# Performance work log

Hardware: AMD Instinct MI355X
Metric: run time of the kernel (lower is better)

## Reference

```python
import jax, jax.numpy as jnp
import numpy as np

B, S, D = 2, 2048, 1024
H = 16
HD = D // H


def setup_inputs() -> dict:
    key = jax.random.key(0)
    ks = jax.random.split(key, 6)
    X = jax.random.normal(ks[0], (B, S, D), dtype=jnp.float32)
    # Linear weights stored [in, out] so y = x @ W (torch stores transposed).
    sc = 1.0 / np.sqrt(D)
    Wq = jax.random.normal(ks[1], (D, D), dtype=jnp.float32) * sc
    Wk = jax.random.normal(ks[2], (D, D), dtype=jnp.float32) * sc
    Wv = jax.random.normal(ks[3], (D, D), dtype=jnp.float32) * sc
    Wo = jax.random.normal(ks[4], (D, D), dtype=jnp.float32) * sc
    bo = jax.random.normal(ks[5], (D,), dtype=jnp.float32) * 0.01
    return {"X": X, "Wq": Wq, "Wk": Wk, "Wv": Wv, "Wo": Wo, "bo": bo}


def reference(X, Wq, Wk, Wv, Wo, bo):
    b, n, _ = X.shape
    # QKV projections (no bias, qkv_bias=False), reshape to [b, h, n, hd]
    q = (X @ Wq).reshape(b, n, H, HD).transpose(0, 2, 1, 3)
    k = (X @ Wk).reshape(b, n, H, HD).transpose(0, 2, 1, 3)
    v = (X @ Wv).reshape(b, n, H, HD).transpose(0, 2, 1, 3)
    # Unscaled scores (module's scale flag defaults to False)
    scores = jnp.einsum("bhqd,bhkd->bhqk", q, k)
    causal = jnp.triu(jnp.ones((n, n), dtype=bool), k=1)  # True above diagonal
    scores = jnp.where(causal, -jnp.inf, scores)
    attn = jax.nn.softmax(scores, axis=-1)
    # dropout p=0.0 -> identity
    ctx = jnp.einsum("bhqk,bhkd->bqhd", attn, v).reshape(b, n, H * HD)
    return ctx @ Wo + bo
```

## Files before the change

kernel.cpp:

```cpp
#include <hip/hip_runtime.h>
#include <stdint.h>


typedef __attribute__((ext_vector_type(8))) short short8;
typedef __attribute__((ext_vector_type(4))) float floatx4;

#define S_LEN 2048
#define D_DIM 1024
#define NH 16
#define HD 64
#define L2E 1.44269504088896340736f

__device__ __forceinline__ short f2bf(float f) {
    uint32_t u = __builtin_bit_cast(uint32_t, f);
    uint32_t r = u + 0x7fffu + ((u >> 16) & 1u);
    return (short)(r >> 16);
}
__device__ __forceinline__ uint32_t pack2(float a, float b) {
#if __has_builtin(__builtin_amdgcn_cvt_pk_bf16_f32)
    auto v = __builtin_amdgcn_cvt_pk_bf16_f32(a, b);
    uint32_t r; __builtin_memcpy(&r, &v, sizeof(r)); return r;
#else
    return (uint32_t)(uint16_t)f2bf(a) | ((uint32_t)(uint16_t)f2bf(b) << 16);
#endif
}
__device__ __forceinline__ void gll16(const void* g, void* l) {
    __builtin_amdgcn_global_load_lds(
        (const __attribute__((address_space(1))) void*)g,
        (__attribute__((address_space(3))) void*)l, 16, 0, 0);
}

__global__ __launch_bounds__(256) void castx_kernel(const float* __restrict__ X,
                                                    short* __restrict__ Xb) {
    int i = blockIdx.x * 256 + threadIdx.x;
    const float4 v = *(const float4*)(X + (size_t)i * 4);
    uint2 o;
    o.x = pack2(v.x, v.y);
    o.y = pack2(v.z, v.w);
    *(uint2*)(Xb + (size_t)i * 4) = o;
}

__global__ __launch_bounds__(256) void tcast4_kernel(const float* __restrict__ Wq,
                                                     const float* __restrict__ Wk,
                                                     const float* __restrict__ Wv,
                                                     const float* __restrict__ Wo,
                                                     short* __restrict__ WqkvT,
                                                     short* __restrict__ WoT) {
    const int z = blockIdx.z;
    const float* W = (z == 0) ? Wq : (z == 1) ? Wk : (z == 2) ? Wv : Wo;
    short* WT = (z < 3) ? (WqkvT + (size_t)z * 1024 * 1024) : WoT;
    __shared__ float tile[32][33];
    const int bx = blockIdx.x * 32;
    const int by = blockIdx.y * 32;
    const int tx = threadIdx.x, ty = threadIdx.y;
    for (int i = 0; i < 32; i += 8)
        tile[ty + i][tx] = W[(size_t)(bx + ty + i) * D_DIM + by + tx];
    __syncthreads();
    for (int i = 0; i < 32; i += 8)
        WT[(size_t)(by + ty + i) * D_DIM + bx + tx] = f2bf(tile[tx][ty + i]);
}

__device__ __forceinline__ void gemm_main(const short* __restrict__ A,
                                          const short* __restrict__ BT,
                                          short* As, short* Bs,
                                          int m0, int n0, floatx4 (&acc)[4][4],
                                          int tid) {
    const int lane = tid & 63, ln = lane & 15, quad = lane >> 4;
    const int wave = tid >> 6;
    const int mw = (wave & 1) * 64, nw = (wave >> 1) * 64;
    for (int k0 = 0; k0 < D_DIM; k0 += 64) {
        __syncthreads();
        for (int t = 0; t < 4; t++) {
            const int c = t * 256 + tid;
            const int row = c >> 3, pos = c & 7, src = pos ^ (row & 7);
            gll16(A  + (size_t)(m0 + row) * D_DIM + k0 + src * 8, As + c * 8);
            gll16(BT + (size_t)(n0 + row) * D_DIM + k0 + src * 8, Bs + c * 8);
        }
        __syncthreads();
        for (int ks = 0; ks < 2; ks++) {
            short8 a[4], b[4];
            for (int i = 0; i < 4; i++) {
                const int row = mw + i * 16 + ln;
                a[i] = *(const short8*)(As + row * 64 + (((ks * 4 + quad) ^ (ln & 7)) * 8));
            }
            for (int j = 0; j < 4; j++) {
                const int row = nw + j * 16 + ln;
                b[j] = *(const short8*)(Bs + row * 64 + (((ks * 4 + quad) ^ (ln & 7)) * 8));
            }
            for (int i = 0; i < 4; i++)
                for (int j = 0; j < 4; j++)
                    acc[i][j] = __builtin_amdgcn_mfma_f32_16x16x32_bf16(a[i], b[j], acc[i][j], 0, 0, 0);
        }
    }
}

__global__ __launch_bounds__(256) void gemm_qkv_kernel(const short* __restrict__ Xb,
                                                       const short* __restrict__ WT,
                                                       short* __restrict__ Qb,
                                                       short* __restrict__ Kb,
                                                       short* __restrict__ Vtb) {
    __shared__ __align__(16) short As[128 * 64];
    __shared__ __align__(16) short Bs[128 * 64];
    const int m0 = blockIdx.x * 128, n0 = blockIdx.y * 128;
    floatx4 acc[4][4] = {};
    gemm_main(Xb, WT, As, Bs, m0, n0, acc, threadIdx.x);

    const int tid = threadIdx.x, wave = tid >> 6, lane = tid & 63;
    const int ln = lane & 15, quad = lane >> 4;
    const int mw = (wave & 1) * 64, nw = (wave >> 1) * 64;
    const int nsel = n0 >> 10;
    short* outB = (nsel == 0) ? Qb : (nsel == 1 ? Kb : Vtb);
    for (int i = 0; i < 4; i++)
        for (int j = 0; j < 4; j++)
            for (int r = 0; r < 4; r++) {
                const int row = m0 + mw + i * 16 + quad * 4 + r;
                const int col = (n0 & 1023) + nw + j * 16 + ln;
                const int bb = row >> 11, s = row & (S_LEN - 1);
                const int h = col >> 6, hd = col & (HD - 1);
                const short v = f2bf(acc[i][j][r]);
                if (nsel < 2)
                    outB[(((size_t)(bb * NH + h)) * S_LEN + s) * HD + hd] = v;
                else
                    outB[(((size_t)(bb * NH + h)) * HD + hd) * S_LEN + s] = v;
            }
}

__global__ __launch_bounds__(256) void gemm_out_kernel(const short* __restrict__ Cb,
                                                       const short* __restrict__ WoT,
                                                       float* __restrict__ out,
                                                       const float* __restrict__ bias) {
    __shared__ __align__(16) short As[128 * 64];
    __shared__ __align__(16) short Bs[128 * 64];
    const int m0 = blockIdx.x * 128, n0 = blockIdx.y * 128;
    floatx4 acc[4][4] = {};
    gemm_main(Cb, WoT, As, Bs, m0, n0, acc, threadIdx.x);

    const int tid = threadIdx.x, wave = tid >> 6, lane = tid & 63;
    const int ln = lane & 15, quad = lane >> 4;
    const int mw = (wave & 1) * 64, nw = (wave >> 1) * 64;
    for (int i = 0; i < 4; i++)
        for (int j = 0; j < 4; j++)
            for (int r = 0; r < 4; r++) {
                const int row = m0 + mw + i * 16 + quad * 4 + r;
                const int col = n0 + nw + j * 16 + ln;
                out[(size_t)row * D_DIM + col] = acc[i][j][r] + bias[col];
            }
}

__global__ __launch_bounds__(256) void attn_kernel(const short* __restrict__ Q,
                                                   const short* __restrict__ Kg,
                                                   const short* __restrict__ Vt,
                                                   short* __restrict__ ctx,
                                                   float* __restrict__ Opart,
                                                   float* __restrict__ Mlpart) {
    __shared__ __align__(16) short Ks[64 * 64];
    __shared__ __align__(16) short Vs[64 * 64];
    __shared__ __align__(16) short Ps[4][16 * 72];

    const int tid = threadIdx.x, wave = tid >> 6, lane = tid & 63;
    const int ln = lane & 15, quad = lane >> 4;

    const int id = blockIdx.x;
    const int xcd = id & 7;
    const int j = id >> 3;
    const int bh = xcd + 8 * (j & 3);
    const int t = j >> 2;
    int qt, k_begin, k_end, pidx;
    if (t < 32) {
        qt = 31 - (t >> 1);
        const int half = t & 1;
        const int n = qt + 1, h0 = n >> 1;
        k_begin = half ? h0 : 0;
        k_end   = half ? n  : h0;
        pidx = ((qt - 16) * 32 + bh) * 2 + half;
    } else {
        qt = 47 - t;
        k_begin = 0; k_end = qt + 1;
        pidx = -1;
    }
    const int q0 = qt * 64;
    const int bb = bh >> 4, h = bh & 15;

    const short* qrow = Q + ((size_t)bh * S_LEN + q0 + wave * 16 + ln) * HD;
    const short8 qb0 = *(const short8*)(qrow + quad * 8);
    const short8 qb1 = *(const short8*)(qrow + 32 + quad * 8);

    float m_run = -INFINITY, l_run = 0.f;
    floatx4 o_acc[4] = {};

    for (int kt = k_begin; kt < k_end; kt++) {
        const int k0 = kt * 64;
        __syncthreads();
        for (int tt = 0; tt < 2; tt++) {
            const int c = tt * 256 + tid;
            const int row = c >> 3, pos = c & 7, src = pos ^ (row & 7);
            gll16(Kg + ((size_t)bh * S_LEN + k0 + row) * HD + src * 8, Ks + c * 8);
            gll16(Vt + ((size_t)bh * HD + row) * S_LEN + k0 + src * 8, Vs + c * 8);
        }
        __syncthreads();

        floatx4 sc[4];
        for (int nt = 0; nt < 4; nt++) {
            const int row = nt * 16 + ln;
            const short8 ak0 = *(const short8*)(Ks + row * 64 + ((quad ^ (ln & 7)) * 8));
            const short8 ak1 = *(const short8*)(Ks + row * 64 + (((quad + 4) ^ (ln & 7)) * 8));
            floatx4 z = {};
            z = __builtin_amdgcn_mfma_f32_16x16x32_bf16(ak0, qb0, z, 0, 0, 0);
            z = __builtin_amdgcn_mfma_f32_16x16x32_bf16(ak1, qb1, z, 0, 0, 0);
            sc[nt] = z;
        }

        if (kt == qt) {
            const int q_abs = q0 + wave * 16 + ln;
            for (int nt = 0; nt < 4; nt++)
                for (int r = 0; r < 4; r++)
                    if (k0 + nt * 16 + quad * 4 + r > q_abs) sc[nt][r] = -1e30f;
        }

        float mt = sc[0][0];
        for (int nt = 0; nt < 4; nt++)
            for (int r = 0; r < 4; r++) mt = fmaxf(mt, sc[nt][r]);
        mt = fmaxf(mt, __shfl_xor(mt, 16, 64));
        mt = fmaxf(mt, __shfl_xor(mt, 32, 64));
        const float mnew = fmaxf(m_run, mt);
        const float alpha = exp2f((m_run - mnew) * L2E);
        float pv[4][4], ls = 0.f;
        for (int nt = 0; nt < 4; nt++)
            for (int r = 0; r < 4; r++) {
                const float e = exp2f((sc[nt][r] - mnew) * L2E);
                pv[nt][r] = e; ls += e;
            }
        ls += __shfl_xor(ls, 16, 64);
        ls += __shfl_xor(ls, 32, 64);
        l_run = l_run * alpha + ls;
        m_run = mnew;
        for (int dt = 0; dt < 4; dt++)
            for (int r = 0; r < 4; r++) o_acc[dt][r] *= alpha;

        for (int nt = 0; nt < 4; nt++) {
            uint2 u;
            u.x = pack2(pv[nt][0], pv[nt][1]);
            u.y = pack2(pv[nt][2], pv[nt][3]);
            *(uint2*)&Ps[wave][ln * 72 + nt * 16 + quad * 4] = u;
        }
        const short8 bp0 = *(const short8*)&Ps[wave][ln * 72 + quad * 8];
        const short8 bp1 = *(const short8*)&Ps[wave][ln * 72 + 32 + quad * 8];

        for (int dt = 0; dt < 4; dt++) {
            const int row = dt * 16 + ln;
            const short8 av0 = *(const short8*)(Vs + row * 64 + ((quad ^ (ln & 7)) * 8));
            const short8 av1 = *(const short8*)(Vs + row * 64 + (((quad + 4) ^ (ln & 7)) * 8));
            o_acc[dt] = __builtin_amdgcn_mfma_f32_16x16x32_bf16(av0, bp0, o_acc[dt], 0, 0, 0);
            o_acc[dt] = __builtin_amdgcn_mfma_f32_16x16x32_bf16(av1, bp1, o_acc[dt], 0, 0, 0);
        }
    }

    if (pidx >= 0) {
        float* Ob = Opart + (size_t)pidx * 4096 + (wave * 16 + ln) * 64;
        for (int dt = 0; dt < 4; dt++)
            *(float4*)(Ob + dt * 16 + quad * 4) = *(float4*)&o_acc[dt];
        if (quad == 0) {
            Mlpart[(size_t)pidx * 128 + wave * 16 + ln]      = m_run;
            Mlpart[(size_t)pidx * 128 + 64 + wave * 16 + ln] = l_run;
        }
    } else {
        const float rl = 1.f / l_run;
        for (int dt = 0; dt < 4; dt++) {
            uint2 u;
            u.x = pack2(o_acc[dt][0] * rl, o_acc[dt][1] * rl);
            u.y = pack2(o_acc[dt][2] * rl, o_acc[dt][3] * rl);
            *(uint2*)&Ps[wave][ln * 72 + dt * 16 + quad * 4] = u;
        }
        const int qr = lane >> 2, sg = lane & 3;
        for (int c = 0; c < 2; c++) {
            const short8 v = *(const short8*)&Ps[wave][qr * 72 + sg * 8 + c * 32];
            const int s = q0 + wave * 16 + qr;
            *(short8*)(ctx + ((size_t)bb * S_LEN + s) * D_DIM + h * HD + sg * 8 + c * 32) = v;
        }
    }
}

__global__ __launch_bounds__(256) void combine_kernel(const float* __restrict__ Opart,
                                                      const float* __restrict__ Mlpart,
                                                      short* __restrict__ ctx) {
    const int tile = blockIdx.x;
    const int qt = 16 + (tile >> 5), bh = tile & 31;
    const int bb = bh >> 4, h = bh & 15;
    const int p0 = ((qt - 16) * 32 + bh) * 2;
    const float* O0 = Opart + (size_t)p0 * 4096;
    const float* O1 = O0 + 4096;
    const float* ml0 = Mlpart + (size_t)p0 * 128;
    const float* ml1 = ml0 + 128;
    for (int e = threadIdx.x; e < 1024; e += 256) {
        const int q = e >> 4, dseg = e & 15;
        const float m0 = ml0[q], l0 = ml0[64 + q];
        const float m1 = ml1[q], l1 = ml1[64 + q];
        const float m = fmaxf(m0, m1);
        const float a0 = exp2f((m0 - m) * L2E), a1 = exp2f((m1 - m) * L2E);
        const float rl = 1.f / (l0 * a0 + l1 * a1);
        const float4 x0 = *(const float4*)(O0 + q * 64 + dseg * 4);
        const float4 x1 = *(const float4*)(O1 + q * 64 + dseg * 4);
        uint2 u;
        u.x = pack2((x0.x * a0 + x1.x * a1) * rl, (x0.y * a0 + x1.y * a1) * rl);
        u.y = pack2((x0.z * a0 + x1.z * a1) * rl, (x0.w * a0 + x1.w * a1) * rl);
        const int s = qt * 64 + q;
        *(uint2*)(ctx + ((size_t)bb * S_LEN + s) * D_DIM + h * HD + dseg * 4) = u;
    }
}

extern "C" void kernel_launch(void* const* d_in, const int* in_sizes, int n_in,
                              void* d_out, int out_size, void* d_ws, size_t ws_size,
                              hipStream_t stream) {
    const float* X  = (const float*)d_in[0];
    const float* Wq = (const float*)d_in[1];
    const float* Wk = (const float*)d_in[2];
    const float* Wv = (const float*)d_in[3];
    const float* Wo = (const float*)d_in[4];
    const float* bo = (const float*)d_in[5];
    float* out = (float*)d_out;

    char* ws = (char*)d_ws;
    const size_t MB = 1024 * 1024;
    short* Xb     = (short*)(ws);
    short* WqkvT  = (short*)(ws + 8  * MB);
    short* Qb     = (short*)(ws + 16 * MB);
    short* Kb     = (short*)(ws + 24 * MB);
    short* Vtb    = (short*)(ws + 32 * MB);
    short* ctxb   = (short*)(ws + 40 * MB);
    short* WoT    = (short*)(ws + 48 * MB);
    float* Opart  = (float*)(ws);
    float* Mlpart = (float*)(ws + 50 * MB);

    castx_kernel<<<4096, 256, 0, stream>>>(X, Xb);
    dim3 tg(32, 32, 4), tb(32, 8);
    tcast4_kernel<<<tg, tb, 0, stream>>>(Wq, Wk, Wv, Wo, WqkvT, WoT);

    dim3 gq(32, 24);
    gemm_qkv_kernel<<<gq, 256, 0, stream>>>(Xb, WqkvT, Qb, Kb, Vtb);

    attn_kernel<<<1536, 256, 0, stream>>>(Qb, Kb, Vtb, ctxb, Opart, Mlpart);
    combine_kernel<<<512, 256, 0, stream>>>(Opart, Mlpart, ctxb);

    dim3 go(32, 8);
    gemm_out_kernel<<<go, 256, 0, stream>>>(ctxb, WoT, out, bo);
}
```

Before: 199.8 us.

## Stage QKV epilogue through LDS, fold log2e into Q, widen attention key tiles

The QKV GEMM epilogue now stages results in shared memory and writes coalesced 16-byte rows, including a transposed V layout. It also pre-multiplies Q by log2(e) so the softmax can call exp2 directly. The attention kernel processes 128-key tiles instead of 64, skips the rescale when no row max changes (ballot), and sets a 3-blocks-per-CU launch bound. The intent is to cut scattered 2-byte global stores, per-iteration sync and softmax overhead, at the cost of more LDS and registers per block and a coarser causal split.

```diff
diff --git a/kernel.cpp b/kernel.cpp
--- a/kernel.cpp
+++ b/kernel.cpp
@@ -99,8 +99,9 @@
                                                        short* __restrict__ Qb,
                                                        short* __restrict__ Kb,
                                                        short* __restrict__ Vtb) {
-    __shared__ __align__(16) short As[128 * 64];
-    __shared__ __align__(16) short Bs[128 * 64];
+    __shared__ __align__(16) short LB[2 * 128 * 64];
+    short* As = LB;
+    short* Bs = LB + 128 * 64;
     const int m0 = blockIdx.x * 128, n0 = blockIdx.y * 128;
     floatx4 acc[4][4] = {};
     gemm_main(Xb, WT, As, Bs, m0, n0, acc, threadIdx.x);
@@ -109,28 +110,52 @@
     const int ln = lane & 15, quad = lane >> 4;
     const int mw = (wave & 1) * 64, nw = (wave >> 1) * 64;
     const int nsel = n0 >> 10;
-    short* outB = (nsel == 0) ? Qb : (nsel == 1 ? Kb : Vtb);
-    for (int i = 0; i < 4; i++)
-        for (int j = 0; j < 4; j++)
-            for (int r = 0; r < 4; r++) {
-                const int row = m0 + mw + i * 16 + quad * 4 + r;
-                const int col = (n0 & 1023) + nw + j * 16 + ln;
-                const int bb = row >> 11, s = row & (S_LEN - 1);
-                const int h = col >> 6, hd = col & (HD - 1);
-                const short v = f2bf(acc[i][j][r]);
-                if (nsel < 2)
-                    outB[(((size_t)(bb * NH + h)) * S_LEN + s) * HD + hd] = v;
-                else
-                    outB[(((size_t)(bb * NH + h)) * HD + hd) * S_LEN + s] = v;
-            }
+    const int hb = (n0 & 1023) >> 6;
+    const int bb = m0 >> 11, s0 = m0 & (S_LEN - 1);
+    short* T = LB;
+
+    __syncthreads();
+    if (nsel < 2) {
+        const float qs = (nsel == 0) ? L2E : 1.f;
+        for (int i = 0; i < 4; i++)
+            for (int j = 0; j < 4; j++)
+                for (int r = 0; r < 4; r++)
+                    T[(mw + i * 16 + quad * 4 + r) * 128 + nw + j * 16 + ln] =
+                        f2bf(acc[i][j][r] * qs);
+        __syncthreads();
+        short* outB = (nsel == 0) ? Qb : Kb;
+        for (int it = 0; it < 8; it++) {
+            const int g = it * 256 + tid;
+            const int tl = g >> 4, hh = (g >> 3) & 1, sg = g & 7;
+            const short8 v = *(const short8*)(T + tl * 128 + hh * 64 + sg * 8);
+            *(short8*)(outB + (((size_t)(bb * NH + hb + hh)) * S_LEN + s0 + tl) * HD + sg * 8) = v;
+        }
+    } else {
+        for (int i = 0; i < 4; i++)
+            for (int j = 0; j < 4; j++) {
+                uint2 u;
+                u.x = pack2(acc[i][j][0], acc[i][j][1]);
+                u.y = pack2(acc[i][j][2], acc[i][j][3]);
+                *(uint2*)(T + (nw + j * 16 + ln) * 128 + mw + i * 16 + quad * 4) = u;
+            }
+        __syncthreads();
+        for (int it = 0; it < 8; it++) {
+            const int g = it * 256 + tid;
+            const int f = g >> 4, tc = g & 15;
+            const short8 v = *(const short8*)(T + f * 128 + tc * 8);
+            *(short8*)(Vtb + (((size_t)(bb * NH + hb + (f >> 6))) * HD + (f & 63)) * S_LEN
+                       + s0 + tc * 8) = v;
+        }
+    }
 }
 
 __global__ __launch_bounds__(256) void gemm_out_kernel(const short* __restrict__ Cb,
                                                        const short* __restrict__ WoT,
                                                        float* __restrict__ out,
                                                        const float* __restrict__ bias) {
-    __shared__ __align__(16) short As[128 * 64];
-    __shared__ __align__(16) short Bs[128 * 64];
+    __shared__ __align__(16) short LB[2 * 128 * 64];
+    short* As = LB;
+    short* Bs = LB + 128 * 64;
     const int m0 = blockIdx.x * 128, n0 = blockIdx.y * 128;
     floatx4 acc[4][4] = {};
     gemm_main(Cb, WoT, As, Bs, m0, n0, acc, threadIdx.x);
@@ -147,111 +172,121 @@
             }
 }
 
-__global__ __launch_bounds__(256) void attn_kernel(const short* __restrict__ Q,
-                                                   const short* __restrict__ Kg,
-                                                   const short* __restrict__ Vt,
-                                                   short* __restrict__ ctx,
-                                                   float* __restrict__ Opart,
-                                                   float* __restrict__ Mlpart) {
-    __shared__ __align__(16) short Ks[64 * 64];
-    __shared__ __align__(16) short Vs[64 * 64];
-    __shared__ __align__(16) short Ps[4][16 * 72];
+#define PST 136
+
+__global__ __launch_bounds__(256, 3) void attn_kernel(const short* __restrict__ Q,
+                                                      const short* __restrict__ Kg,
+                                                      const short* __restrict__ Vt,
+                                                      short* __restrict__ ctx,
+                                                      float* __restrict__ Opart,
+                                                      float* __restrict__ Mlpart) {
+    __shared__ __align__(16) short Ks[128 * 64];
+    __shared__ __align__(16) short Vs[64 * 128];
+    __shared__ __align__(16) short Ps[4][16 * PST];
 
     const int tid = threadIdx.x, wave = tid >> 6, lane = tid & 63;
     const int ln = lane & 15, quad = lane >> 4;
 
     const int id = blockIdx.x;
-    const int xcd = id & 7;
-    const int j = id >> 3;
-    const int bh = xcd + 8 * (j & 3);
-    const int t = j >> 2;
+    const int bh = (id & 7) + 8 * ((id >> 3) & 3);
+    const int t = id >> 5;
     int qt, k_begin, k_end, pidx;
     if (t < 32) {
         qt = 31 - (t >> 1);
         const int half = t & 1;
-        const int n = qt + 1, h0 = n >> 1;
+        const int n = (qt + 2) >> 1;
+        const int h0 = n >> 1;
         k_begin = half ? h0 : 0;
         k_end   = half ? n  : h0;
         pidx = ((qt - 16) * 32 + bh) * 2 + half;
     } else {
         qt = 47 - t;
-        k_begin = 0; k_end = qt + 1;
+        k_begin = 0; k_end = (qt + 2) >> 1;
         pidx = -1;
     }
+    const int kmask = ((qt + 2) >> 1) - 1;
     const int q0 = qt * 64;
     const int bb = bh >> 4, h = bh & 15;
+    short* Pw = &Ps[wave][0];
 
     const short* qrow = Q + ((size_t)bh * S_LEN + q0 + wave * 16 + ln) * HD;
     const short8 qb0 = *(const short8*)(qrow + quad * 8);
     const short8 qb1 = *(const short8*)(qrow + 32 + quad * 8);
+    const int q_abs = q0 + wave * 16 + ln;
 
     float m_run = -INFINITY, l_run = 0.f;
     floatx4 o_acc[4] = {};
 
     for (int kt = k_begin; kt < k_end; kt++) {
-        const int k0 = kt * 64;
-        __syncthreads();
-        for (int tt = 0; tt < 2; tt++) {
+        const int k0 = kt * 128;
+        __syncthreads();
+        for (int tt = 0; tt < 4; tt++) {
             const int c = tt * 256 + tid;
-            const int row = c >> 3, pos = c & 7, src = pos ^ (row & 7);
-            gll16(Kg + ((size_t)bh * S_LEN + k0 + row) * HD + src * 8, Ks + c * 8);
-            gll16(Vt + ((size_t)bh * HD + row) * S_LEN + k0 + src * 8, Vs + c * 8);
-        }
-        __syncthreads();
-
-        floatx4 sc[4];
-        for (int nt = 0; nt < 4; nt++) {
+            {
+                const int row = c >> 3, pos = c & 7, src = pos ^ (row & 7);
+                gll16(Kg + ((size_t)bh * S_LEN + k0 + row) * HD + src * 8, Ks + c * 8);
+            }
+            {
+                const int row = c >> 4, pos = c & 15, src = pos ^ (row & 15);
+                gll16(Vt + ((size_t)bh * HD + row) * S_LEN + k0 + src * 8, Vs + c * 8);
+            }
+        }
+        __syncthreads();
+
+        floatx4 sc[8];
+        for (int nt = 0; nt < 8; nt++) {
             const int row = nt * 16 + ln;
             const short8 ak0 = *(const short8*)(Ks + row * 64 + ((quad ^ (ln & 7)) * 8));
-            const short8 ak1 = *(const short8*)(Ks + row * 64 + (((quad + 4) ^ (ln & 7)) * 8));
+            const short8 ak1 = *(const short8*)(Ks + row * 64 + (((4 + quad) ^ (ln & 7)) * 8));
             floatx4 z = {};
             z = __builtin_amdgcn_mfma_f32_16x16x32_bf16(ak0, qb0, z, 0, 0, 0);
             z = __builtin_amdgcn_mfma_f32_16x16x32_bf16(ak1, qb1, z, 0, 0, 0);
             sc[nt] = z;
         }
 
-        if (kt == qt) {
-            const int q_abs = q0 + wave * 16 + ln;
-            for (int nt = 0; nt < 4; nt++)
+        if (kt == kmask) {
+            for (int nt = 0; nt < 8; nt++)
                 for (int r = 0; r < 4; r++)
                     if (k0 + nt * 16 + quad * 4 + r > q_abs) sc[nt][r] = -1e30f;
         }
 
         float mt = sc[0][0];
-        for (int nt = 0; nt < 4; nt++)
+        for (int nt = 0; nt < 8; nt++)
             for (int r = 0; r < 4; r++) mt = fmaxf(mt, sc[nt][r]);
         mt = fmaxf(mt, __shfl_xor(mt, 16, 64));
         mt = fmaxf(mt, __shfl_xor(mt, 32, 64));
         const float mnew = fmaxf(m_run, mt);
-        const float alpha = exp2f((m_run - mnew) * L2E);
-        float pv[4][4], ls = 0.f;
-        for (int nt = 0; nt < 4; nt++)
+        if (__ballot(mnew > m_run)) {
+            const float alpha = exp2f(m_run - mnew);
+            l_run *= alpha;
+            for (int dt = 0; dt < 4; dt++)
+                for (int r = 0; r < 4; r++) o_acc[dt][r] *= alpha;
+            m_run = mnew;
+        }
+        float ls = 0.f;
+        for (int nt = 0; nt < 8; nt++)
             for (int r = 0; r < 4; r++) {
-                const float e = exp2f((sc[nt][r] - mnew) * L2E);
-                pv[nt][r] = e; ls += e;
+                const float e = exp2f(sc[nt][r] - m_run);
+                sc[nt][r] = e; ls += e;
             }
         ls += __shfl_xor(ls, 16, 64);
         ls += __shfl_xor(ls, 32, 64);
-        l_run = l_run * alpha + ls;
-        m_run = mnew;
-        for (int dt = 0; dt < 4; dt++)
-            for (int r = 0; r < 4; r++) o_acc[dt][r] *= alpha;
-
-        for (int nt = 0; nt < 4; nt++) {
+        l_run += ls;
+
+        for (int nt = 0; nt < 8; nt++) {
             uint2 u;
-            u.x = pack2(pv[nt][0], pv[nt][1]);
-            u.y = pack2(pv[nt][2], pv[nt][3]);
-            *(uint2*)&Ps[wave][ln * 72 + nt * 16 + quad * 4] = u;
-        }
-        const short8 bp0 = *(const short8*)&Ps[wave][ln * 72 + quad * 8];
-        const short8 bp1 = *(const short8*)&Ps[wave][ln * 72 + 32 + quad * 8];
-
-        for (int dt = 0; dt < 4; dt++) {
-            const int row = dt * 16 + ln;
-            const short8 av0 = *(const short8*)(Vs + row * 64 + ((quad ^ (ln & 7)) * 8));
-            const short8 av1 = *(const short8*)(Vs + row * 64 + (((quad + 4) ^ (ln & 7)) * 8));
-            o_acc[dt] = __builtin_amdgcn_mfma_f32_16x16x32_bf16(av0, bp0, o_acc[dt], 0, 0, 0);
-            o_acc[dt] = __builtin_amdgcn_mfma_f32_16x16x32_bf16(av1, bp1, o_acc[dt], 0, 0, 0);
+            u.x = pack2(sc[nt][0], sc[nt][1]);
+            u.y = pack2(sc[nt][2], sc[nt][3]);
+            *(uint2*)&Pw[ln * PST + nt * 16 + quad * 4] = u;
+        }
+
+        for (int ks = 0; ks < 4; ks++) {
+            const short8 bp = *(const short8*)&Pw[ln * PST + ks * 32 + quad * 8];
+            for (int dt = 0; dt < 4; dt++) {
+                const int row = dt * 16 + ln;
+                const short8 av = *(const short8*)(Vs + row * 128 + (((ks * 4 + quad) ^ (ln & 15)) * 8));
+                o_acc[dt] = __builtin_amdgcn_mfma_f32_16x16x32_bf16(av, bp, o_acc[dt], 0, 0, 0);
+            }
         }
     }
 
@@ -269,11 +304,11 @@
             uint2 u;
             u.x = pack2(o_acc[dt][0] * rl, o_acc[dt][1] * rl);
             u.y = pack2(o_acc[dt][2] * rl, o_acc[dt][3] * rl);
-            *(uint2*)&Ps[wave][ln * 72 + dt * 16 + quad * 4] = u;
+            *(uint2*)&Pw[ln * PST + dt * 16 + quad * 4] = u;
         }
         const int qr = lane >> 2, sg = lane & 3;
         for (int c = 0; c < 2; c++) {
-            const short8 v = *(const short8*)&Ps[wave][qr * 72 + sg * 8 + c * 32];
+            const short8 v = *(const short8*)&Pw[qr * PST + sg * 8 + c * 32];
             const int s = q0 + wave * 16 + qr;
             *(short8*)(ctx + ((size_t)bb * S_LEN + s) * D_DIM + h * HD + sg * 8 + c * 32) = v;
         }
@@ -296,7 +331,7 @@
         const float m0 = ml0[q], l0 = ml0[64 + q];
         const float m1 = ml1[q], l1 = ml1[64 + q];
         const float m = fmaxf(m0, m1);
-        const float a0 = exp2f((m0 - m) * L2E), a1 = exp2f((m1 - m) * L2E);
+        const float a0 = exp2f(m0 - m), a1 = exp2f(m1 - m);
         const float rl = 1.f / (l0 * a0 + l1 * a1);
         const float4 x0 = *(const float4*)(O0 + q * 64 + dseg * 4);
         const float4 x1 = *(const float4*)(O1 + q * 64 + dseg * 4);
```

Result: no change. 203.0 us (+1.6%).
